# Kernel optimization log

Hardware: AMD Instinct MI355X
Metric: run time of the kernel (lower is better)

The kernel has to match this reference:

```python
import jax, jax.numpy as jnp
import numpy as np

B, N, H, HEADS, L, V, T = 4, 256, 256, 4, 128, 256, 100
FF = 4 * H

def _ln(x, g, b, eps=1e-5):
    m = jnp.mean(x, -1, keepdims=True)
    v = jnp.mean((x - m) ** 2, -1, keepdims=True)
    return (x - m) / jnp.sqrt(v + eps) * g + b

def _mha(h, w_qkv, b_qkv, w_o, b_o):
    b, n, hd = h.shape
    d = hd // HEADS
    q, k, v = jnp.split(h @ w_qkv + b_qkv, 3, axis=-1)
    q = q.reshape(b, n, HEADS, d)
    k = k.reshape(b, n, HEADS, d)
    v = v.reshape(b, n, HEADS, d)
    s = jnp.einsum('bihd,bjhd->bhij', q, k) / jnp.sqrt(jnp.float32(d))
    a = jax.nn.softmax(s, axis=-1)
    o = jnp.einsum('bhij,bjhd->bihd', a, v).reshape(b, n, hd)
    return o @ w_o + b_o

def _edge_logits(h, w1, b1, w2, b2):
    # concat([h_i, h_j], -1) @ w1 == h_i @ w1[:H] + h_j @ w1[H:]  (avoids (B,N,N,2H) materialization)
    hi = h @ w1[:H]
    hj = h @ w1[H:]
    pre = hi[:, :, None, :] + hj[:, None, :, :] + b1  # (B,N,N,H)
    return (jax.nn.gelu(pre, approximate=False) @ w2 + b2)[..., 0]

def _gnn_block(x, nbr, qw, qb, kw, kb, vw, vb, sw, sb, l1g, l1b, f1w, f1b, f2w, f2b, l2g, l2b):
    # TransformerConv (PyG, concat=True, root_weight=True) as dense masked attention over in-neighbors.
    b, n, hd = x.shape
    d = hd // HEADS
    q = (x @ qw + qb).reshape(b, n, HEADS, d)
    k = (x @ kw + kb).reshape(b, n, HEADS, d)
    v = (x @ vw + vb).reshape(b, n, HEADS, d)
    s = jnp.einsum('bihd,bjhd->bhij', q, k) / jnp.sqrt(jnp.float32(d))
    m = nbr[:, None, :, :]  # (B,1,N,N); nbr[b,i,j]=True iff edge j->i
    a = jax.nn.softmax(jnp.where(m, s, -1e30), axis=-1) * m  # no-neighbor rows aggregate to 0
    agg = jnp.einsum('bhij,bjhd->bihd', a, v).reshape(b, n, hd)
    x = _ln(x + agg + x @ sw + sb, l1g, l1b)
    ffn = jax.nn.gelu(x @ f1w + f1b, approximate=False) @ f2w + f2b
    return _ln(x + ffn, l2g, l2b)

def _forward(noisy_tokens, t, z, lp1_w, lp1_b, lp2_w, lp2_b, tok_emb, time_tab, time_w, time_b, pos_tab, enc_qkv_w, enc_qkv_b, enc_o_w, enc_o_b, enc_ln1_g, enc_ln1_b, enc_f1_w, enc_f1_b, enc_f2_w, enc_f2_b, enc_ln2_g, enc_ln2_b, gq_w, gq_b, gk_w, gk_b, gv_w, gv_b, gs_w, gs_b, g_ln1_g, g_ln1_b, g_f1_w, g_f1_b, g_f2_w, g_f2_b, g_ln2_g, g_ln2_b, nh1_w, nh1_b, nh2_w, nh2_b, eh1_w, eh1_b, eh2_w, eh2_b, sh1_w, sh1_b, sh2_w, sh2_b):
    lat = jax.nn.relu(z @ lp1_w + lp1_b) @ lp2_w + lp2_b  # (B,H)
    time_e = jax.nn.gelu(time_tab[t] @ time_w + time_b, approximate=False)  # (B,H)
    h = tok_emb[noisy_tokens] + time_e[:, None, :] + pos_tab[None, :, :] + lat[:, None, :]
    for l in range(2):  # post-norm TransformerEncoderLayer, relu FFN
        h = _ln(h + _mha(h, enc_qkv_w[l], enc_qkv_b[l], enc_o_w[l], enc_o_b[l]), enc_ln1_g[l], enc_ln1_b[l])
        h = _ln(h + jax.nn.relu(h @ enc_f1_w[l] + enc_f1_b[l]) @ enc_f2_w[l] + enc_f2_b[l], enc_ln2_g[l], enc_ln2_b[l])
    el0 = _edge_logits(h, eh1_w, eh1_b, eh2_w, eh2_b)
    nbr = jnp.swapaxes(jax.nn.sigmoid(el0) > 0.3, 1, 2)  # transpose: adj[j,i] -> in-neighbors of i
    x = h
    for l in range(4):
        x = _gnn_block(x, nbr, gq_w[l], gq_b[l], gk_w[l], gk_b[l], gv_w[l], gv_b[l], gs_w[l], gs_b[l], g_ln1_g[l], g_ln1_b[l], g_f1_w[l], g_f1_b[l], g_f2_w[l], g_f2_b[l], g_ln2_g[l], g_ln2_b[l])
    node_logits = jax.nn.gelu(x @ nh1_w + nh1_b, approximate=False) @ nh2_w + nh2_b
    edge_logits = _edge_logits(x, eh1_w, eh1_b, eh2_w, eh2_b)
    size_logits = jax.nn.relu(lat @ sh1_w + sh1_b) @ sh2_w + sh2_b
    return node_logits, edge_logits, size_logits

def setup_inputs():
    key = jax.random.key(0)
    ks = iter(jax.random.split(key, 70))
    def p(shape):
        return jax.random.normal(next(ks), shape, dtype=jnp.float32) * 0.02
    return {
        'z': jax.random.normal(next(ks), (B, L), dtype=jnp.float32),
        'noisy_tokens': jax.random.randint(next(ks), (B, N), 0, V),
        't': jax.random.randint(next(ks), (B,), 0, T),
        'lp1_w': p((L, H)), 'lp1_b': p((H,)), 'lp2_w': p((H, H)), 'lp2_b': p((H,)),
        'tok_emb': p((V, H)), 'time_tab': p((T, H)), 'time_w': p((H, H)), 'time_b': p((H,)),
        'pos_tab': p((N, H)),
        'enc_qkv_w': p((2, H, 3 * H)), 'enc_qkv_b': p((2, 3 * H)),
        'enc_o_w': p((2, H, H)), 'enc_o_b': p((2, H)),
        'enc_ln1_g': jnp.ones((2, H)), 'enc_ln1_b': jnp.zeros((2, H)),
        'enc_f1_w': p((2, H, FF)), 'enc_f1_b': p((2, FF)),
        'enc_f2_w': p((2, FF, H)), 'enc_f2_b': p((2, H)),
        'enc_ln2_g': jnp.ones((2, H)), 'enc_ln2_b': jnp.zeros((2, H)),
        'gq_w': p((4, H, H)), 'gq_b': p((4, H)),
        'gk_w': p((4, H, H)), 'gk_b': p((4, H)),
        'gv_w': p((4, H, H)), 'gv_b': p((4, H)),
        'gs_w': p((4, H, H)), 'gs_b': p((4, H)),
        'g_ln1_g': jnp.ones((4, H)), 'g_ln1_b': jnp.zeros((4, H)),
        'g_f1_w': p((4, H, FF)), 'g_f1_b': p((4, FF)),
        'g_f2_w': p((4, FF, H)), 'g_f2_b': p((4, H)),
        'g_ln2_g': jnp.ones((4, H)), 'g_ln2_b': jnp.zeros((4, H)),
        'nh1_w': p((H, H)), 'nh1_b': p((H,)),
        'nh2_w': p((H, V)), 'nh2_b': p((V,)),
        'eh1_w': p((2 * H, H)), 'eh1_b': p((H,)),
        'eh2_w': p((H, 1)), 'eh2_b': p((1,)),
        'sh1_w': p((H, H // 2)), 'sh1_b': p((H // 2,)),
        'sh2_w': p((H // 2, N)), 'sh2_b': p((N,)),
    }

def reference(z, noisy_tokens, t, lp1_w, lp1_b, lp2_w, lp2_b, tok_emb, time_tab, time_w, time_b, pos_tab, enc_qkv_w, enc_qkv_b, enc_o_w, enc_o_b, enc_ln1_g, enc_ln1_b, enc_f1_w, enc_f1_b, enc_f2_w, enc_f2_b, enc_ln2_g, enc_ln2_b, gq_w, gq_b, gk_w, gk_b, gv_w, gv_b, gs_w, gs_b, g_ln1_g, g_ln1_b, g_f1_w, g_f1_b, g_f2_w, g_f2_b, g_ln2_g, g_ln2_b, nh1_w, nh1_b, nh2_w, nh2_b, eh1_w, eh1_b, eh2_w, eh2_b, sh1_w, sh1_b, sh2_w, sh2_b):
    return _forward(noisy_tokens, t, z, lp1_w, lp1_b, lp2_w, lp2_b, tok_emb, time_tab, time_w, time_b, pos_tab, enc_qkv_w, enc_qkv_b, enc_o_w, enc_o_b, enc_ln1_g, enc_ln1_b, enc_f1_w, enc_f1_b, enc_f2_w, enc_f2_b, enc_ln2_g, enc_ln2_b, gq_w, gq_b, gk_w, gk_b, gv_w, gv_b, gs_w, gs_b, g_ln1_g, g_ln1_b, g_f1_w, g_f1_b, g_f2_w, g_f2_b, g_ln2_g, g_ln2_b, nh1_w, nh1_b, nh2_w, nh2_b, eh1_w, eh1_b, eh2_w, eh2_b, sh1_w, sh1_b, sh2_w, sh2_b)
```

## Files before the change

kernel.cpp:

```cpp
#include <hip/hip_runtime.h>
#include <math.h>


typedef __attribute__((ext_vector_type(8))) short bf16x8;
typedef __attribute__((ext_vector_type(4))) float f32x4;

__device__ __forceinline__ unsigned short f2b(float f) {
    unsigned u = __float_as_uint(f);
    u += 0x7FFFu + ((u >> 16) & 1u);
    return (unsigned short)(u >> 16);
}
__device__ __forceinline__ unsigned pack2(float a, float b) {
    return (unsigned)f2b(a) | ((unsigned)f2b(b) << 16);
}
__device__ __forceinline__ bf16x8 as_frag(uint4 v) {
    union { uint4 u; bf16x8 f; } x; x.u = v; return x.f;
}

__device__ __forceinline__ float gelu_f(float x) {
    const float y  = 0.70710678118654752f * x;
    const float ay = fabsf(y);
    const float t  = __builtin_amdgcn_rcpf(fmaf(0.3275911f, ay, 1.0f));
    float S = fmaf(t, 1.061405429f, -1.453152027f);
    S = fmaf(t, S, 1.421413741f);
    S = fmaf(t, S, -0.284496736f);
    S = fmaf(t, S, 0.254829592f);
    S = S * t;
    const float e = __expf(-ay * ay);
    const float E = fmaf(-S, e, 1.0f);
    return 0.5f * x * (1.0f + copysignf(E, y));
}

struct PrepEnt { const float* src; unsigned dstOff; int K; int N; unsigned tstart; };
struct PrepTab { int n; PrepEnt e[36]; };

__global__ __launch_bounds__(256) void k_prep(PrepTab tab, unsigned short* __restrict__ wt)
{
    const int bx = blockIdx.x;
    int ei = 0;
    for (int i = 0; i < tab.n; ++i) if (tab.e[i].tstart <= (unsigned)bx) ei = i;
    const PrepEnt E = tab.e[ei];
    const int tIdx = bx - E.tstart;
    const int ntn = E.N >> 6;
    const int kt = tIdx / ntn, nt = tIdx % ntn;
    const int tid = threadIdx.x;
    __shared__ unsigned Tl[64][36];
    {
        const int r = tid >> 2, c = (tid & 3) * 16;
        const float* s = E.src + (size_t)(kt * 64 + r) * E.N + nt * 64 + c;
        unsigned o[8];
        #pragma unroll
        for (int q = 0; q < 4; ++q) {
            const float4 v = *(const float4*)(s + q * 4);
            o[q * 2 + 0] = pack2(v.x, v.y);
            o[q * 2 + 1] = pack2(v.z, v.w);
        }
        *(uint4*)&Tl[r][c / 2 + 0] = make_uint4(o[0], o[1], o[2], o[3]);
        *(uint4*)&Tl[r][c / 2 + 4] = make_uint4(o[4], o[5], o[6], o[7]);
    }
    __syncthreads();
    {
        const int rn = tid >> 2, ck = (tid & 3) * 16;
        const int sh = (rn & 1) * 16, hw = rn >> 1;
        unsigned o[8];
        #pragma unroll
        for (int s = 0; s < 8; ++s) {
            const unsigned lo = (Tl[ck + 2 * s][hw] >> sh) & 0xFFFFu;
            const unsigned hi = (Tl[ck + 2 * s + 1][hw] >> sh) & 0xFFFFu;
            o[s] = lo | (hi << 16);
        }
        unsigned short* d = wt + E.dstOff + (size_t)(nt * 64 + rn) * E.K + kt * 64 + ck;
        *(uint4*)(d + 0) = make_uint4(o[0], o[1], o[2], o[3]);
        *(uint4*)(d + 8) = make_uint4(o[4], o[5], o[6], o[7]);
    }
}

__device__ __forceinline__ void gemm_mfma_body(
    const float* __restrict__ A, const unsigned short* __restrict__ Wt,
    const float* __restrict__ bias, float* __restrict__ C,
    int K, int ldc, int act, int m0, int n0)
{
    __shared__ unsigned As_u[64][20];
    __shared__ unsigned Bs_u[64][20];
    const int tid = threadIdx.x;
    const int arow = tid >> 2, ac = tid & 3;
    const float* ap = A + (size_t)(m0 + arow) * K + ac * 8;
    const unsigned short* bp = Wt + (size_t)(n0 + arow) * K + ac * 8;
    float4 av0 = *(const float4*)ap;
    float4 av1 = *(const float4*)(ap + 4);
    uint4  bv  = *(const uint4*)bp;
    f32x4 acc00 = {0.f,0.f,0.f,0.f}, acc01 = acc00, acc10 = acc00, acc11 = acc00;
    const int l = tid & 63, wid = tid >> 6;
    const int wm = wid & 1, wn = wid >> 1, lr = l & 15, lg = l >> 4;
    for (int k0 = 0; k0 < K; k0 += 32) {
        *(uint4*)&As_u[arow][ac * 4] = make_uint4(pack2(av0.x, av0.y), pack2(av0.z, av0.w),
                                                  pack2(av1.x, av1.y), pack2(av1.z, av1.w));
        *(uint4*)&Bs_u[arow][ac * 4] = bv;
        __syncthreads();
        if (k0 + 32 < K) {
            av0 = *(const float4*)(ap + k0 + 32);
            av1 = *(const float4*)(ap + k0 + 36);
            bv  = *(const uint4*)(bp + k0 + 32);
        }
        const bf16x8 fa0 = as_frag(*(const uint4*)&As_u[wm * 32 + lr][lg * 4]);
        const bf16x8 fa1 = as_frag(*(const uint4*)&As_u[wm * 32 + 16 + lr][lg * 4]);
        const bf16x8 fb0 = as_frag(*(const uint4*)&Bs_u[wn * 32 + lr][lg * 4]);
        const bf16x8 fb1 = as_frag(*(const uint4*)&Bs_u[wn * 32 + 16 + lr][lg * 4]);
        acc00 = __builtin_amdgcn_mfma_f32_16x16x32_bf16(fa0, fb0, acc00, 0, 0, 0);
        acc01 = __builtin_amdgcn_mfma_f32_16x16x32_bf16(fa0, fb1, acc01, 0, 0, 0);
        acc10 = __builtin_amdgcn_mfma_f32_16x16x32_bf16(fa1, fb0, acc10, 0, 0, 0);
        acc11 = __builtin_amdgcn_mfma_f32_16x16x32_bf16(fa1, fb1, acc11, 0, 0, 0);
        __syncthreads();
    }
    const int cb0 = n0 + wn * 32 + lr, cb1 = cb0 + 16;
    const float b0 = bias ? bias[cb0] : 0.f;
    const float b1 = bias ? bias[cb1] : 0.f;
    #pragma unroll
    for (int r = 0; r < 4; ++r) {
        const int row0 = m0 + wm * 32 + lg * 4 + r;
        const int row1 = row0 + 16;
        float v00 = acc00[r] + b0, v01 = acc01[r] + b1;
        float v10 = acc10[r] + b0, v11 = acc11[r] + b1;
        if (act == 1) {
            v00 = fmaxf(v00, 0.f); v01 = fmaxf(v01, 0.f);
            v10 = fmaxf(v10, 0.f); v11 = fmaxf(v11, 0.f);
        } else if (act == 2) {
            v00 = gelu_f(v00); v01 = gelu_f(v01);
            v10 = gelu_f(v10); v11 = gelu_f(v11);
        }
        C[(size_t)row0 * ldc + cb0] = v00;
        C[(size_t)row0 * ldc + cb1] = v01;
        C[(size_t)row1 * ldc + cb0] = v10;
        C[(size_t)row1 * ldc + cb1] = v11;
    }
}

__global__ __launch_bounds__(256) void k_gemm_mfma(
    const float* __restrict__ A, const unsigned short* __restrict__ Wt,
    const float* __restrict__ bias, float* __restrict__ C, int K, int ldc, int act)
{
    gemm_mfma_body(A, Wt, bias, C, K, ldc, act, blockIdx.y * 64, blockIdx.x * 64);
}

struct MW4 { const unsigned short* wt[4]; const float* b[4]; };
__global__ __launch_bounds__(256) void k_gemm_mfma4(
    const float* __restrict__ A, MW4 p, float* __restrict__ C)
{
    const int z = blockIdx.z;
    gemm_mfma_body(A, p.wt[z], p.b[z], C + z * 256, 256, 1024, 0,
                   blockIdx.y * 64, blockIdx.x * 64);
}

__global__ __launch_bounds__(256) void k_mv(
    const float* __restrict__ A, const int* __restrict__ aidx, int K,
    const float* __restrict__ W, const float* __restrict__ bias,
    float* __restrict__ out, int N, int act)
{
    const int r = blockIdx.x, c0 = blockIdx.y * 64;
    const int c = threadIdx.x & 63, ks = threadIdx.x >> 6;
    const float* arow = A + (size_t)(aidx ? aidx[r] : r) * K;
    float s = 0.f;
    for (int k = ks; k < K; k += 4) s += arow[k] * W[(size_t)k * N + c0 + c];
    __shared__ float red[4][64];
    red[ks][c] = s;
    __syncthreads();
    if (ks == 0) {
        float v = red[0][c] + red[1][c] + red[2][c] + red[3][c] + (bias ? bias[c0 + c] : 0.f);
        if (act == 1) v = fmaxf(v, 0.f); else if (act == 2) v = gelu_f(v);
        out[(size_t)r * N + c0 + c] = v;
    }
}

__global__ __launch_bounds__(256) void k_embed(
    const int* __restrict__ tok, const float* __restrict__ tok_emb,
    const float* __restrict__ pos, const float* __restrict__ lat,
    const float* __restrict__ te, float* __restrict__ h)
{
    const int r = blockIdx.x, c = threadIdx.x;
    const int b = r >> 8, n = r & 255;
    h[(size_t)r * 256 + c] = tok_emb[(size_t)tok[r] * 256 + c] + te[b * 256 + c]
                           + pos[n * 256 + c] + lat[b * 256 + c];
}

__global__ __launch_bounds__(256) void k_attn2(
    const float* __restrict__ qkv, int ld, int qo, int ko, int vo,
    const unsigned char* __restrict__ mask, float* __restrict__ out)
{
    const int blk = blockIdx.x;
    const int ig = blk & 15, hh = (blk >> 4) & 3, b = blk >> 6;
    const int i0 = ig * 16;
    const int t = threadIdx.x;
    __shared__ float Qs[16][68];
    __shared__ float Ts[64][68];
    __shared__ float Ss[16][260];

    {
        const int r = t >> 4, c = (t & 15) * 4;
        *(float4*)&Qs[r][c] = *(const float4*)&qkv[(size_t)(b * 256 + i0 + r) * ld + qo + hh * 64 + c];
    }
    const int i = t >> 4, tx = t & 15;

    for (int jt = 0; jt < 4; ++jt) {
        __syncthreads();
        {
            const int jr = t >> 2, cs = (t & 3) * 16;
            const float* src = &qkv[(size_t)(b * 256 + jt * 64 + jr) * ld + ko + hh * 64 + cs];
            *(float4*)&Ts[jr][cs + 0]  = *(const float4*)(src + 0);
            *(float4*)&Ts[jr][cs + 4]  = *(const float4*)(src + 4);
            *(float4*)&Ts[jr][cs + 8]  = *(const float4*)(src + 8);
            *(float4*)&Ts[jr][cs + 12] = *(const float4*)(src + 12);
        }
        __syncthreads();
        float s0 = 0.f, s1 = 0.f, s2 = 0.f, s3 = 0.f;
        #pragma unroll 8
        for (int d = 0; d < 64; ++d) {
            const float qd = Qs[i][d];
            s0 += qd * Ts[tx][d];
            s1 += qd * Ts[tx + 16][d];
            s2 += qd * Ts[tx + 32][d];
            s3 += qd * Ts[tx + 48][d];
        }
        Ss[i][jt * 64 + tx]      = s0;
        Ss[i][jt * 64 + tx + 16] = s1;
        Ss[i][jt * 64 + tx + 32] = s2;
        Ss[i][jt * 64 + tx + 48] = s3;
    }

    {
        const unsigned char* mrow = mask ? &mask[(size_t)(b * 256 + i0 + i) * 256] : nullptr;
        float sv[16]; bool okv[16];
        float m = -3.0e38f;
        #pragma unroll
        for (int k = 0; k < 16; ++k) {
            const int j = tx + 16 * k;
            const float s = Ss[i][j] * 0.125f;
            const bool ok = mrow ? (mrow[j] != 0) : true;
            sv[k] = s; okv[k] = ok;
            if (ok) m = fmaxf(m, s);
        }
        #pragma unroll
        for (int w = 1; w < 16; w <<= 1) m = fmaxf(m, __shfl_xor(m, w, 64));
        float ev[16]; float sum = 0.f;
        #pragma unroll
        for (int k = 0; k < 16; ++k) {
            ev[k] = okv[k] ? __expf(sv[k] - m) : 0.f;
            sum += ev[k];
        }
        #pragma unroll
        for (int w = 1; w < 16; w <<= 1) sum += __shfl_xor(sum, w, 64);
        const float inv = (sum > 0.f) ? 1.f / sum : 0.f;
        #pragma unroll
        for (int k = 0; k < 16; ++k) Ss[i][tx + 16 * k] = ev[k] * inv;
    }

    const int d4 = tx * 4;
    float4 o = {0.f, 0.f, 0.f, 0.f};
    for (int jt = 0; jt < 4; ++jt) {
        __syncthreads();
        {
            const int jr = t >> 2, cs = (t & 3) * 16;
            const float* src = &qkv[(size_t)(b * 256 + jt * 64 + jr) * ld + vo + hh * 64 + cs];
            *(float4*)&Ts[jr][cs + 0]  = *(const float4*)(src + 0);
            *(float4*)&Ts[jr][cs + 4]  = *(const float4*)(src + 4);
            *(float4*)&Ts[jr][cs + 8]  = *(const float4*)(src + 8);
            *(float4*)&Ts[jr][cs + 12] = *(const float4*)(src + 12);
        }
        __syncthreads();
        #pragma unroll 8
        for (int j = 0; j < 64; ++j) {
            const float p = Ss[i][jt * 64 + j];
            const float4 v4 = *(const float4*)&Ts[j][d4];
            o.x += p * v4.x; o.y += p * v4.y; o.z += p * v4.z; o.w += p * v4.w;
        }
    }
    *(float4*)&out[(size_t)(b * 256 + i0 + i) * 256 + hh * 64 + d4] = o;
}

__global__ __launch_bounds__(256) void k_ln(
    const float* __restrict__ a, const float* __restrict__ bb, int ldb,
    const float* __restrict__ cc, int ldc,
    const float* __restrict__ g, const float* __restrict__ beta, float* __restrict__ out)
{
    const int r = blockIdx.x, t = threadIdx.x;
    float v = a[(size_t)r * 256 + t];
    if (bb) v += bb[(size_t)r * ldb + t];
    if (cc) v += cc[(size_t)r * ldc + t];
    __shared__ float rs[256], rq[256];
    rs[t] = v; rq[t] = v * v;
    __syncthreads();
    for (int off = 128; off > 0; off >>= 1) {
        if (t < off) { rs[t] += rs[t + off]; rq[t] += rq[t + off]; }
        __syncthreads();
    }
    const float mean = rs[0] * (1.0f / 256.0f);
    const float var  = rq[0] * (1.0f / 256.0f) - mean * mean;
    out[(size_t)r * 256 + t] = (v - mean) * rsqrtf(var + 1e-5f) * g[t] + beta[t];
}

__global__ __launch_bounds__(256) void k_edge2(
    const float* __restrict__ hi, const float* __restrict__ hj,
    const float* __restrict__ w2, const float* __restrict__ b2,
    float* __restrict__ val_out, unsigned char* __restrict__ mask_out)
{
    const int jg = blockIdx.x, ig = blockIdx.y, b = blockIdx.z;
    const int t = threadIdx.x;
    __shared__ float his[16][260];
    __shared__ float hjs[16][260];
    __shared__ float w2s[256];
    {
        const int r = t >> 4, c = (t & 15) * 16;
        const float* s1 = &hi[(size_t)(b * 256 + ig * 16 + r) * 256 + c];
        const float* s2 = &hj[(size_t)(b * 256 + jg * 16 + r) * 256 + c];
        #pragma unroll
        for (int q = 0; q < 4; ++q) {
            *(float4*)&his[r][c + q * 4] = *(const float4*)(s1 + q * 4);
            *(float4*)&hjs[r][c + q * 4] = *(const float4*)(s2 + q * 4);
        }
        w2s[t] = w2[t];
    }
    __syncthreads();
    const int i = t >> 4, j = t & 15;
    float acc = 0.f;
    #pragma unroll 4
    for (int h = 0; h < 256; ++h) acc += gelu_f(his[i][h] + hjs[j][h]) * w2s[h];
    const float v = acc + b2[0];
    if (val_out)  val_out[(size_t)b * 65536 + (ig * 16 + i) * 256 + jg * 16 + j] = v;
    if (mask_out) mask_out[(size_t)b * 65536 + (jg * 16 + j) * 256 + ig * 16 + i] =
                      (v > -0.84729786038720f) ? 1 : 0;
}

extern "C" void kernel_launch(void* const* d_in, const int* in_sizes, int n_in,
                              void* d_out, int out_size, void* d_ws, size_t ws_size,
                              hipStream_t stream) {
    const float* z     = (const float*)d_in[0];
    const int*   tok   = (const int*)d_in[1];
    const int*   tt    = (const int*)d_in[2];
    const float* lp1w  = (const float*)d_in[3];
    const float* lp1b  = (const float*)d_in[4];
    const float* lp2w  = (const float*)d_in[5];
    const float* lp2b  = (const float*)d_in[6];
    const float* temb  = (const float*)d_in[7];
    const float* ttab  = (const float*)d_in[8];
    const float* tw    = (const float*)d_in[9];
    const float* tb    = (const float*)d_in[10];
    const float* pos   = (const float*)d_in[11];
    const float* qkvw  = (const float*)d_in[12];
    const float* qkvb  = (const float*)d_in[13];
    const float* ow    = (const float*)d_in[14];
    const float* ob    = (const float*)d_in[15];
    const float* ln1g  = (const float*)d_in[16];
    const float* ln1b  = (const float*)d_in[17];
    const float* f1w   = (const float*)d_in[18];
    const float* f1b   = (const float*)d_in[19];
    const float* f2w   = (const float*)d_in[20];
    const float* f2b   = (const float*)d_in[21];
    const float* ln2g  = (const float*)d_in[22];
    const float* ln2b  = (const float*)d_in[23];
    const float* gqw   = (const float*)d_in[24];
    const float* gqb   = (const float*)d_in[25];
    const float* gkw   = (const float*)d_in[26];
    const float* gkb   = (const float*)d_in[27];
    const float* gvw   = (const float*)d_in[28];
    const float* gvb   = (const float*)d_in[29];
    const float* gsw   = (const float*)d_in[30];
    const float* gsb   = (const float*)d_in[31];
    const float* gl1g  = (const float*)d_in[32];
    const float* gl1b  = (const float*)d_in[33];
    const float* gf1w  = (const float*)d_in[34];
    const float* gf1b  = (const float*)d_in[35];
    const float* gf2w  = (const float*)d_in[36];
    const float* gf2b  = (const float*)d_in[37];
    const float* gl2g  = (const float*)d_in[38];
    const float* gl2b  = (const float*)d_in[39];
    const float* nh1w  = (const float*)d_in[40];
    const float* nh1b  = (const float*)d_in[41];
    const float* nh2w  = (const float*)d_in[42];
    const float* nh2b  = (const float*)d_in[43];
    const float* eh1w  = (const float*)d_in[44];
    const float* eh1b  = (const float*)d_in[45];
    const float* eh2w  = (const float*)d_in[46];
    const float* eh2b  = (const float*)d_in[47];
    const float* sh1w  = (const float*)d_in[48];
    const float* sh1b  = (const float*)d_in[49];
    const float* sh2w  = (const float*)d_in[50];
    const float* sh2b  = (const float*)d_in[51];

    float* W = (float*)d_ws;
    float* Hh  = W + 0;
    float* QK  = W + 262144;
    float* AO  = W + 1310720;
    float* T1  = W + 1572864;
    float* HI  = W + 1835008;
    float* HJ  = W + 2097152;
    float* LAT = W + 2359296;
    float* TE  = W + 2360320;
    float* A1  = W + 2361344;
    float* SH  = W + 2362368;
    unsigned char* MASK = (unsigned char*)(W + 2362880);
    unsigned short* wt  = (unsigned short*)(W + 2428416);

    float* out      = (float*)d_out;
    float* out_node = out;
    float* out_edge = out + 262144;
    float* out_sz   = out + 524288;

    PrepTab tab; int ne = 0; unsigned tiles = 0;
    auto add = [&](const float* src, int K, int N, unsigned off) {
        tab.e[ne].src = src; tab.e[ne].K = K; tab.e[ne].N = N;
        tab.e[ne].dstOff = off; tab.e[ne].tstart = tiles;
        tiles += (unsigned)((K >> 6) * (N >> 6)); ++ne;
    };
    for (int l = 0; l < 2; ++l) add(qkvw + (size_t)l * 196608, 256, 768,  0 + l * 196608);
    for (int l = 0; l < 2; ++l) add(ow   + (size_t)l * 65536,  256, 256,  393216 + l * 65536);
    for (int l = 0; l < 2; ++l) add(f1w  + (size_t)l * 262144, 256, 1024, 524288 + l * 262144);
    for (int l = 0; l < 2; ++l) add(f2w  + (size_t)l * 262144, 1024, 256, 1048576 + l * 262144);
    for (int l = 0; l < 4; ++l) add(gqw  + (size_t)l * 65536,  256, 256,  1572864 + l * 65536);
    for (int l = 0; l < 4; ++l) add(gkw  + (size_t)l * 65536,  256, 256,  1835008 + l * 65536);
    for (int l = 0; l < 4; ++l) add(gvw  + (size_t)l * 65536,  256, 256,  2097152 + l * 65536);
    for (int l = 0; l < 4; ++l) add(gsw  + (size_t)l * 65536,  256, 256,  2359296 + l * 65536);
    for (int l = 0; l < 4; ++l) add(gf1w + (size_t)l * 262144, 256, 1024, 2621440 + l * 262144);
    for (int l = 0; l < 4; ++l) add(gf2w + (size_t)l * 262144, 1024, 256, 3670016 + l * 262144);
    add(nh1w, 256, 256, 4718592);
    add(nh2w, 256, 256, 4784128);
    add(eh1w,         256, 256, 4849664);
    add(eh1w + 65536, 256, 256, 4915200);
    tab.n = ne;
    k_prep<<<tiles, 256, 0, stream>>>(tab, wt);

    auto gemmM = [&](const float* Aa, size_t wtoff, const float* bias, float* Cc,
                     int M, int N, int K, int ldc, int act) {
        k_gemm_mfma<<<dim3(N / 64, M / 64), 256, 0, stream>>>(Aa, wt + wtoff, bias, Cc, K, ldc, act);
    };

    k_mv<<<dim3(4, 4), 256, 0, stream>>>(z,    nullptr, 128, lp1w, lp1b, A1,     256, 1);
    k_mv<<<dim3(4, 4), 256, 0, stream>>>(ttab, tt,      256, tw,   tb,   TE,     256, 2);
    k_mv<<<dim3(4, 4), 256, 0, stream>>>(A1,   nullptr, 256, lp2w, lp2b, LAT,    256, 0);
    k_mv<<<dim3(4, 2), 256, 0, stream>>>(LAT,  nullptr, 256, sh1w, sh1b, SH,     128, 1);
    k_mv<<<dim3(4, 4), 256, 0, stream>>>(SH,   nullptr, 128, sh2w, sh2b, out_sz, 256, 0);

    k_embed<<<1024, 256, 0, stream>>>(tok, temb, pos, LAT, TE, Hh);

    for (int l = 0; l < 2; ++l) {
        gemmM(Hh, (size_t)l * 196608, qkvb + l * 768, QK, 1024, 768, 256, 768, 0);
        k_attn2<<<256, 256, 0, stream>>>(QK, 768, 0, 256, 512, nullptr, AO);
        gemmM(AO, 393216 + (size_t)l * 65536, ob + l * 256, T1, 1024, 256, 256, 256, 0);
        k_ln<<<1024, 256, 0, stream>>>(Hh, T1, 256, nullptr, 0, ln1g + l * 256, ln1b + l * 256, Hh);
        gemmM(Hh, 524288 + (size_t)l * 262144, f1b + l * 1024, QK, 1024, 1024, 256, 1024, 1);
        gemmM(QK, 1048576 + (size_t)l * 262144, f2b + l * 256, T1, 1024, 256, 1024, 256, 0);
        k_ln<<<1024, 256, 0, stream>>>(Hh, T1, 256, nullptr, 0, ln2g + l * 256, ln2b + l * 256, Hh);
    }

    gemmM(Hh, 4849664, eh1b, HI, 1024, 256, 256, 256, 0);
    gemmM(Hh, 4915200, nullptr, HJ, 1024, 256, 256, 256, 0);
    k_edge2<<<dim3(16, 16, 4), 256, 0, stream>>>(HI, HJ, eh2w, eh2b, nullptr, MASK);

    for (int l = 0; l < 4; ++l) {
        MW4 p;
        p.wt[0] = wt + 1572864 + (size_t)l * 65536; p.b[0] = gqb + l * 256;
        p.wt[1] = wt + 1835008 + (size_t)l * 65536; p.b[1] = gkb + l * 256;
        p.wt[2] = wt + 2097152 + (size_t)l * 65536; p.b[2] = gvb + l * 256;
        p.wt[3] = wt + 2359296 + (size_t)l * 65536; p.b[3] = gsb + l * 256;
        k_gemm_mfma4<<<dim3(4, 16, 4), 256, 0, stream>>>(Hh, p, QK);
        k_attn2<<<256, 256, 0, stream>>>(QK, 1024, 0, 256, 512, MASK, AO);
        k_ln<<<1024, 256, 0, stream>>>(Hh, AO, 256, QK + 768, 1024, gl1g + l * 256, gl1b + l * 256, Hh);
        gemmM(Hh, 2621440 + (size_t)l * 262144, gf1b + l * 1024, QK, 1024, 1024, 256, 1024, 2);
        gemmM(QK, 3670016 + (size_t)l * 262144, gf2b + l * 256, T1, 1024, 256, 1024, 256, 0);
        k_ln<<<1024, 256, 0, stream>>>(Hh, T1, 256, nullptr, 0, gl2g + l * 256, gl2b + l * 256, Hh);
    }

    gemmM(Hh, 4718592, nh1b, T1, 1024, 256, 256, 256, 2);
    gemmM(T1, 4784128, nh2b, out_node, 1024, 256, 256, 256, 0);
    gemmM(Hh, 4849664, eh1b, HI, 1024, 256, 256, 256, 0);
    gemmM(Hh, 4915200, nullptr, HJ, 1024, 256, 256, 256, 0);
    k_edge2<<<dim3(16, 16, 4), 256, 0, stream>>>(HI, HJ, eh2w, eh2b, out_edge, nullptr);
}
```

Measured before the change: 733.7 us.

## Load MFMA fragments directly from global, add 32x32 GEMM tiles, shuffle-based LayerNorm

The GEMM kernels drop the shared-memory staging and barriers. Each wave now loads its bf16 fragments straight from global memory, converting the fp32 A operand to bf16 in registers. A new 32x32-tile variant is used for the N=256 GEMMs so more blocks fill the GPU, and LayerNorm becomes one wavefront per row with float4 loads and xor-shuffle reductions. The edge kernel gets vectorised shared reads and padded rows. Operands are no longer reused across waves through shared memory, so redundant global and L2 traffic goes up.

Result: slower. 750.0 us (+2.2%).

```diff
diff --git a/kernel.cpp b/kernel.cpp
--- a/kernel.cpp
+++ b/kernel.cpp
@@ -15,6 +15,14 @@
 }
 __device__ __forceinline__ bf16x8 as_frag(uint4 v) {
     union { uint4 u; bf16x8 f; } x; x.u = v; return x.f;
+}
+__device__ __forceinline__ bf16x8 ld_frag_f32(const float* p) {
+    const float4 v0 = *(const float4*)p;
+    const float4 v1 = *(const float4*)(p + 4);
+    union { unsigned u[4]; bf16x8 f; } x;
+    x.u[0] = pack2(v0.x, v0.y); x.u[1] = pack2(v0.z, v0.w);
+    x.u[2] = pack2(v1.x, v1.y); x.u[3] = pack2(v1.z, v1.w);
+    return x.f;
 }
 
 __device__ __forceinline__ float gelu_f(float x) {
@@ -75,52 +83,40 @@
     }
 }
 
-__device__ __forceinline__ void gemm_mfma_body(
+
+__device__ __forceinline__ void gd64_body(
     const float* __restrict__ A, const unsigned short* __restrict__ Wt,
     const float* __restrict__ bias, float* __restrict__ C,
     int K, int ldc, int act, int m0, int n0)
 {
-    __shared__ unsigned As_u[64][20];
-    __shared__ unsigned Bs_u[64][20];
     const int tid = threadIdx.x;
-    const int arow = tid >> 2, ac = tid & 3;
-    const float* ap = A + (size_t)(m0 + arow) * K + ac * 8;
-    const unsigned short* bp = Wt + (size_t)(n0 + arow) * K + ac * 8;
-    float4 av0 = *(const float4*)ap;
-    float4 av1 = *(const float4*)(ap + 4);
-    uint4  bv  = *(const uint4*)bp;
-    f32x4 acc00 = {0.f,0.f,0.f,0.f}, acc01 = acc00, acc10 = acc00, acc11 = acc00;
     const int l = tid & 63, wid = tid >> 6;
     const int wm = wid & 1, wn = wid >> 1, lr = l & 15, lg = l >> 4;
+    const float* a0 = A + (size_t)(m0 + wm * 32 + lr) * K + lg * 8;
+    const float* a1 = a0 + (size_t)16 * K;
+    const unsigned short* b0 = Wt + (size_t)(n0 + wn * 32 + lr) * K + lg * 8;
+    const unsigned short* b1 = b0 + (size_t)16 * K;
+    f32x4 acc00 = {0.f,0.f,0.f,0.f}, acc01 = acc00, acc10 = acc00, acc11 = acc00;
+    #pragma unroll 2
     for (int k0 = 0; k0 < K; k0 += 32) {
-        *(uint4*)&As_u[arow][ac * 4] = make_uint4(pack2(av0.x, av0.y), pack2(av0.z, av0.w),
-                                                  pack2(av1.x, av1.y), pack2(av1.z, av1.w));
-        *(uint4*)&Bs_u[arow][ac * 4] = bv;
-        __syncthreads();
-        if (k0 + 32 < K) {
-            av0 = *(const float4*)(ap + k0 + 32);
-            av1 = *(const float4*)(ap + k0 + 36);
-            bv  = *(const uint4*)(bp + k0 + 32);
-        }
-        const bf16x8 fa0 = as_frag(*(const uint4*)&As_u[wm * 32 + lr][lg * 4]);
-        const bf16x8 fa1 = as_frag(*(const uint4*)&As_u[wm * 32 + 16 + lr][lg * 4]);
-        const bf16x8 fb0 = as_frag(*(const uint4*)&Bs_u[wn * 32 + lr][lg * 4]);
-        const bf16x8 fb1 = as_frag(*(const uint4*)&Bs_u[wn * 32 + 16 + lr][lg * 4]);
+        const bf16x8 fa0 = ld_frag_f32(a0 + k0);
+        const bf16x8 fa1 = ld_frag_f32(a1 + k0);
+        const bf16x8 fb0 = as_frag(*(const uint4*)(b0 + k0));
+        const bf16x8 fb1 = as_frag(*(const uint4*)(b1 + k0));
         acc00 = __builtin_amdgcn_mfma_f32_16x16x32_bf16(fa0, fb0, acc00, 0, 0, 0);
         acc01 = __builtin_amdgcn_mfma_f32_16x16x32_bf16(fa0, fb1, acc01, 0, 0, 0);
         acc10 = __builtin_amdgcn_mfma_f32_16x16x32_bf16(fa1, fb0, acc10, 0, 0, 0);
         acc11 = __builtin_amdgcn_mfma_f32_16x16x32_bf16(fa1, fb1, acc11, 0, 0, 0);
-        __syncthreads();
     }
     const int cb0 = n0 + wn * 32 + lr, cb1 = cb0 + 16;
-    const float b0 = bias ? bias[cb0] : 0.f;
-    const float b1 = bias ? bias[cb1] : 0.f;
+    const float bv0 = bias ? bias[cb0] : 0.f;
+    const float bv1 = bias ? bias[cb1] : 0.f;
     #pragma unroll
     for (int r = 0; r < 4; ++r) {
         const int row0 = m0 + wm * 32 + lg * 4 + r;
         const int row1 = row0 + 16;
-        float v00 = acc00[r] + b0, v01 = acc01[r] + b1;
-        float v10 = acc10[r] + b0, v11 = acc11[r] + b1;
+        float v00 = acc00[r] + bv0, v01 = acc01[r] + bv1;
+        float v10 = acc10[r] + bv0, v11 = acc11[r] + bv1;
         if (act == 1) {
             v00 = fmaxf(v00, 0.f); v01 = fmaxf(v01, 0.f);
             v10 = fmaxf(v10, 0.f); v11 = fmaxf(v11, 0.f);
@@ -135,20 +131,55 @@
     }
 }
 
-__global__ __launch_bounds__(256) void k_gemm_mfma(
+__global__ __launch_bounds__(256) void k_gd64(
     const float* __restrict__ A, const unsigned short* __restrict__ Wt,
     const float* __restrict__ bias, float* __restrict__ C, int K, int ldc, int act)
 {
-    gemm_mfma_body(A, Wt, bias, C, K, ldc, act, blockIdx.y * 64, blockIdx.x * 64);
+    gd64_body(A, Wt, bias, C, K, ldc, act, blockIdx.y * 64, blockIdx.x * 64);
+}
+
+__device__ __forceinline__ void gd32_body(
+    const float* __restrict__ A, const unsigned short* __restrict__ Wt,
+    const float* __restrict__ bias, float* __restrict__ C,
+    int K, int ldc, int act, int m0, int n0)
+{
+    const int tid = threadIdx.x;
+    const int l = tid & 63, wid = tid >> 6;
+    const int qm = wid & 1, qn = wid >> 1, lr = l & 15, lg = l >> 4;
+    const float* ap = A + (size_t)(m0 + qm * 16 + lr) * K + lg * 8;
+    const unsigned short* bp = Wt + (size_t)(n0 + qn * 16 + lr) * K + lg * 8;
+    f32x4 acc = {0.f,0.f,0.f,0.f};
+    #pragma unroll 4
+    for (int k0 = 0; k0 < K; k0 += 32) {
+        const bf16x8 fa = ld_frag_f32(ap + k0);
+        const bf16x8 fb = as_frag(*(const uint4*)(bp + k0));
+        acc = __builtin_amdgcn_mfma_f32_16x16x32_bf16(fa, fb, acc, 0, 0, 0);
+    }
+    const int cc = n0 + qn * 16 + lr;
+    const float bv = bias ? bias[cc] : 0.f;
+    #pragma unroll
+    for (int r = 0; r < 4; ++r) {
+        const int row = m0 + qm * 16 + lg * 4 + r;
+        float v = acc[r] + bv;
+        if (act == 1) v = fmaxf(v, 0.f); else if (act == 2) v = gelu_f(v);
+        C[(size_t)row * ldc + cc] = v;
+    }
+}
+
+__global__ __launch_bounds__(256) void k_gd32(
+    const float* __restrict__ A, const unsigned short* __restrict__ Wt,
+    const float* __restrict__ bias, float* __restrict__ C, int K, int ldc, int act)
+{
+    gd32_body(A, Wt, bias, C, K, ldc, act, blockIdx.y * 32, blockIdx.x * 32);
 }
 
 struct MW4 { const unsigned short* wt[4]; const float* b[4]; };
-__global__ __launch_bounds__(256) void k_gemm_mfma4(
+__global__ __launch_bounds__(256) void k_gd32_4(
     const float* __restrict__ A, MW4 p, float* __restrict__ C)
 {
     const int z = blockIdx.z;
-    gemm_mfma_body(A, p.wt[z], p.b[z], C + z * 256, 256, 1024, 0,
-                   blockIdx.y * 64, blockIdx.x * 64);
+    gd32_body(A, p.wt[z], p.b[z], C + z * 256, 256, 1024, 0,
+              blockIdx.y * 32, blockIdx.x * 32);
 }
 
 __global__ __launch_bounds__(256) void k_mv(
@@ -276,36 +307,51 @@
     *(float4*)&out[(size_t)(b * 256 + i0 + i) * 256 + hh * 64 + d4] = o;
 }
 
-__global__ __launch_bounds__(256) void k_ln(
+__global__ __launch_bounds__(256) void k_ln2(
     const float* __restrict__ a, const float* __restrict__ bb, int ldb,
     const float* __restrict__ cc, int ldc,
     const float* __restrict__ g, const float* __restrict__ beta, float* __restrict__ out)
 {
-    const int r = blockIdx.x, t = threadIdx.x;
-    float v = a[(size_t)r * 256 + t];
-    if (bb) v += bb[(size_t)r * ldb + t];
-    if (cc) v += cc[(size_t)r * ldc + t];
-    __shared__ float rs[256], rq[256];
-    rs[t] = v; rq[t] = v * v;
-    __syncthreads();
-    for (int off = 128; off > 0; off >>= 1) {
-        if (t < off) { rs[t] += rs[t + off]; rq[t] += rq[t + off]; }
-        __syncthreads();
-    }
-    const float mean = rs[0] * (1.0f / 256.0f);
-    const float var  = rq[0] * (1.0f / 256.0f) - mean * mean;
-    out[(size_t)r * 256 + t] = (v - mean) * rsqrtf(var + 1e-5f) * g[t] + beta[t];
-}
-
-__global__ __launch_bounds__(256) void k_edge2(
+    const int r = blockIdx.x * 4 + (threadIdx.x >> 6);
+    const int c4 = (threadIdx.x & 63) * 4;
+    float4 v = *(const float4*)&a[(size_t)r * 256 + c4];
+    if (bb) {
+        const float4 u = *(const float4*)&bb[(size_t)r * ldb + c4];
+        v.x += u.x; v.y += u.y; v.z += u.z; v.w += u.w;
+    }
+    if (cc) {
+        const float4 u = *(const float4*)&cc[(size_t)r * ldc + c4];
+        v.x += u.x; v.y += u.y; v.z += u.z; v.w += u.w;
+    }
+    float s = v.x + v.y + v.z + v.w;
+    float q = v.x * v.x + v.y * v.y + v.z * v.z + v.w * v.w;
+    #pragma unroll
+    for (int w = 1; w < 64; w <<= 1) {
+        s += __shfl_xor(s, w, 64);
+        q += __shfl_xor(q, w, 64);
+    }
+    const float mean = s * (1.0f / 256.0f);
+    const float var  = q * (1.0f / 256.0f) - mean * mean;
+    const float inv  = rsqrtf(var + 1e-5f);
+    const float4 gg = *(const float4*)&g[c4];
+    const float4 be = *(const float4*)&beta[c4];
+    float4 o;
+    o.x = (v.x - mean) * inv * gg.x + be.x;
+    o.y = (v.y - mean) * inv * gg.y + be.y;
+    o.z = (v.z - mean) * inv * gg.z + be.z;
+    o.w = (v.w - mean) * inv * gg.w + be.w;
+    *(float4*)&out[(size_t)r * 256 + c4] = o;
+}
+
+__global__ __launch_bounds__(256) void k_edge3(
     const float* __restrict__ hi, const float* __restrict__ hj,
     const float* __restrict__ w2, const float* __restrict__ b2,
     float* __restrict__ val_out, unsigned char* __restrict__ mask_out)
 {
     const int jg = blockIdx.x, ig = blockIdx.y, b = blockIdx.z;
     const int t = threadIdx.x;
-    __shared__ float his[16][260];
-    __shared__ float hjs[16][260];
+    __shared__ float his[16][268];
+    __shared__ float hjs[16][268];
     __shared__ float w2s[256];
     {
         const int r = t >> 4, c = (t & 15) * 16;
@@ -322,7 +368,15 @@
     const int i = t >> 4, j = t & 15;
     float acc = 0.f;
     #pragma unroll 4
-    for (int h = 0; h < 256; ++h) acc += gelu_f(his[i][h] + hjs[j][h]) * w2s[h];
+    for (int h4 = 0; h4 < 64; ++h4) {
+        const float4 hv  = *(const float4*)&hjs[j][h4 * 4];
+        const float4 hi4 = *(const float4*)&his[i][h4 * 4];
+        const float4 w4  = *(const float4*)&w2s[h4 * 4];
+        acc += gelu_f(hi4.x + hv.x) * w4.x;
+        acc += gelu_f(hi4.y + hv.y) * w4.y;
+        acc += gelu_f(hi4.z + hv.z) * w4.z;
+        acc += gelu_f(hi4.w + hv.w) * w4.w;
+    }
     const float v = acc + b2[0];
     if (val_out)  val_out[(size_t)b * 65536 + (ig * 16 + i) * 256 + jg * 16 + j] = v;
     if (mask_out) mask_out[(size_t)b * 65536 + (jg * 16 + j) * 256 + ig * 16 + i] =
@@ -427,9 +481,13 @@
     tab.n = ne;
     k_prep<<<tiles, 256, 0, stream>>>(tab, wt);
 
-    auto gemmM = [&](const float* Aa, size_t wtoff, const float* bias, float* Cc,
-                     int M, int N, int K, int ldc, int act) {
-        k_gemm_mfma<<<dim3(N / 64, M / 64), 256, 0, stream>>>(Aa, wt + wtoff, bias, Cc, K, ldc, act);
+    auto g64 = [&](const float* Aa, size_t wtoff, const float* bias, float* Cc,
+                   int N, int K, int ldc, int act) {
+        k_gd64<<<dim3(N / 64, 16), 256, 0, stream>>>(Aa, wt + wtoff, bias, Cc, K, ldc, act);
+    };
+    auto g32 = [&](const float* Aa, size_t wtoff, const float* bias, float* Cc,
+                   int K, int ldc, int act) {
+        k_gd32<<<dim3(8, 32), 256, 0, stream>>>(Aa, wt + wtoff, bias, Cc, K, ldc, act);
     };
 
     k_mv<<<dim3(4, 4), 256, 0, stream>>>(z,    nullptr, 128, lp1w, lp1b, A1,     256, 1);
@@ -441,18 +499,18 @@
     k_embed<<<1024, 256, 0, stream>>>(tok, temb, pos, LAT, TE, Hh);
 
     for (int l = 0; l < 2; ++l) {
-        gemmM(Hh, (size_t)l * 196608, qkvb + l * 768, QK, 1024, 768, 256, 768, 0);
+        g64(Hh, (size_t)l * 196608, qkvb + l * 768, QK, 768, 256, 768, 0);
         k_attn2<<<256, 256, 0, stream>>>(QK, 768, 0, 256, 512, nullptr, AO);
-        gemmM(AO, 393216 + (size_t)l * 65536, ob + l * 256, T1, 1024, 256, 256, 256, 0);
-        k_ln<<<1024, 256, 0, stream>>>(Hh, T1, 256, nullptr, 0, ln1g + l * 256, ln1b + l * 256, Hh);
-        gemmM(Hh, 524288 + (size_t)l * 262144, f1b + l * 1024, QK, 1024, 1024, 256, 1024, 1);
-        gemmM(QK, 1048576 + (size_t)l * 262144, f2b + l * 256, T1, 1024, 256, 1024, 256, 0);
-        k_ln<<<1024, 256, 0, stream>>>(Hh, T1, 256, nullptr, 0, ln2g + l * 256, ln2b + l * 256, Hh);
-    }
-
-    gemmM(Hh, 4849664, eh1b, HI, 1024, 256, 256, 256, 0);
-    gemmM(Hh, 4915200, nullptr, HJ, 1024, 256, 256, 256, 0);
-    k_edge2<<<dim3(16, 16, 4), 256, 0, stream>>>(HI, HJ, eh2w, eh2b, nullptr, MASK);
+        g32(AO, 393216 + (size_t)l * 65536, ob + l * 256, T1, 256, 256, 0);
+        k_ln2<<<256, 256, 0, stream>>>(Hh, T1, 256, nullptr, 0, ln1g + l * 256, ln1b + l * 256, Hh);
+        g64(Hh, 524288 + (size_t)l * 262144, f1b + l * 1024, QK, 1024, 256, 1024, 1);
+        g32(QK, 1048576 + (size_t)l * 262144, f2b + l * 256, T1, 1024, 256, 0);
+        k_ln2<<<256, 256, 0, stream>>>(Hh, T1, 256, nullptr, 0, ln2g + l * 256, ln2b + l * 256, Hh);
+    }
+
+    g32(Hh, 4849664, eh1b, HI, 256, 256, 0);
+    g32(Hh, 4915200, nullptr, HJ, 256, 256, 0);
+    k_edge3<<<dim3(16, 16, 4), 256, 0, stream>>>(HI, HJ, eh2w, eh2b, nullptr, MASK);
 
     for (int l = 0; l < 4; ++l) {
         MW4 p;
@@ -460,17 +518,17 @@
         p.wt[1] = wt + 1835008 + (size_t)l * 65536; p.b[1] = gkb + l * 256;
         p.wt[2] = wt + 2097152 + (size_t)l * 65536; p.b[2] = gvb + l * 256;
         p.wt[3] = wt + 2359296 + (size_t)l * 65536; p.b[3] = gsb + l * 256;
-        k_gemm_mfma4<<<dim3(4, 16, 4), 256, 0, stream>>>(Hh, p, QK);
+        k_gd32_4<<<dim3(8, 32, 4), 256, 0, stream>>>(Hh, p, QK);
         k_attn2<<<256, 256, 0, stream>>>(QK, 1024, 0, 256, 512, MASK, AO);
-        k_ln<<<1024, 256, 0, stream>>>(Hh, AO, 256, QK + 768, 1024, gl1g + l * 256, gl1b + l * 256, Hh);
-        gemmM(Hh, 2621440 + (size_t)l * 262144, gf1b + l * 1024, QK, 1024, 1024, 256, 1024, 2);
-        gemmM(QK, 3670016 + (size_t)l * 262144, gf2b + l * 256, T1, 1024, 256, 1024, 256, 0);
-        k_ln<<<1024, 256, 0, stream>>>(Hh, T1, 256, nullptr, 0, gl2g + l * 256, gl2b + l * 256, Hh);
-    }
-
-    gemmM(Hh, 4718592, nh1b, T1, 1024, 256, 256, 256, 2);
-    gemmM(T1, 4784128, nh2b, out_node, 1024, 256, 256, 256, 0);
-    gemmM(Hh, 4849664, eh1b, HI, 1024, 256, 256, 256, 0);
-    gemmM(Hh, 4915200, nullptr, HJ, 1024, 256, 256, 256, 0);
-    k_edge2<<<dim3(16, 16, 4), 256, 0, stream>>>(HI, HJ, eh2w, eh2b, out_edge, nullptr);
-}
+        k_ln2<<<256, 256, 0, stream>>>(Hh, AO, 256, QK + 768, 1024, gl1g + l * 256, gl1b + l * 256, Hh);
+        g64(Hh, 2621440 + (size_t)l * 262144, gf1b + l * 1024, QK, 1024, 256, 1024, 2);
+        g32(QK, 3670016 + (size_t)l * 262144, gf2b + l * 256, T1, 1024, 256, 0);
+        k_ln2<<<256, 256, 0, stream>>>(Hh, T1, 256, nullptr, 0, gl2g + l * 256, gl2b + l * 256, Hh);
+    }
+
+    g32(Hh, 4718592, nh1b, T1, 256, 256, 2);
+    g32(T1, 4784128, nh2b, out_node, 256, 256, 0);
+    g32(Hh, 4849664, eh1b, HI, 256, 256, 0);
+    g32(Hh, 4915200, nullptr, HJ, 256, 256, 0);
+    k_edge3<<<dim3(16, 16, 4), 256, 0, stream>>>(HI, HJ, eh2w, eh2b, out_edge, nullptr);
+}
```
